# Kernel tuning notes

Hardware: AMD Instinct MI355X
Metric: run time of the kernel (lower is better)

## Reference

```python
import jax, jax.numpy as jnp
import numpy as np
import math

HEADS = 8
DIM_HEAD = 64


def setup_inputs() -> dict:
    key = jax.random.key(0)
    k1, k2, k3 = jax.random.split(key, 3)
    b, n, dim = 4, 2048, 512
    inner = HEADS * DIM_HEAD  # 512
    x = jax.random.normal(k1, (b, n, dim), dtype=jnp.float32)
    W_qkv = jax.random.normal(k2, (dim, 4 * inner), dtype=jnp.float32) * (dim ** -0.5)
    W_out = jax.random.normal(k3, (2 * inner, dim), dtype=jnp.float32) * ((2 * inner) ** -0.5)
    b_out = jnp.zeros((dim,), dtype=jnp.float32)
    return {"x": x, "W_qkv": W_qkv, "W_out": W_out, "b_out": b_out}


def reference(x, W_qkv, W_out, b_out):
    b, n, d = x.shape
    h, dh = HEADS, DIM_HEAD
    scale = dh ** -0.5
    qkvt = x @ W_qkv  # [b, n, 4*h*dh]
    q, k, v, t = jnp.split(qkvt, 4, axis=-1)
    # 'b n (h d) -> b h n d'
    def to_heads(z):
        return z.reshape(b, n, h, dh).transpose(0, 2, 1, 3)
    q, k, v, t = map(to_heads, (q, k, v, t))

    # Branch 1: standard softmax attention
    dots = jnp.einsum('bhid,bhjd->bhij', q, k) * scale
    attn1 = jax.nn.softmax(dots, axis=-1)
    out1 = jnp.einsum('bhij,bhjd->bhid', attn1, v)

    # Branch 2: fixed positional-decay attention (shared across b, h; no repeat needed)
    pos = jnp.arange(1, n + 1, dtype=x.dtype)  # linspace(1, n, n)
    tg = jnp.abs(pos[None, :] - pos[:, None])  # |j - i|, [n, n]
    attn2 = jnp.exp(-tg / jnp.asarray(math.e, dtype=x.dtype))
    # NOTE: original divides by sum(-1) WITHOUT keepdim -> broadcasts over columns:
    # attn2[i, j] / sum_k attn2[j, k]
    attn2 = attn2 / attn2.sum(-1)
    out2 = jnp.einsum('ij,bhjd->bhid', attn2, t)

    out = jnp.concatenate([out1, out2], axis=-1)  # [b, h, n, 2*dh]
    out = out.transpose(0, 2, 1, 3).reshape(b, n, 2 * h * dh)  # 'b h n d -> b n (h d)'
    return out @ W_out + b_out
```

## Files before the change

### kernel.cpp

```cpp
#include <hip/hip_runtime.h>
#include <hip/hip_bf16.h>

#define B_ 4
#define N_ 2048
#define D_ 512
#define H_ 8
#define DH_ 64

typedef float float4_ __attribute__((ext_vector_type(4)));
typedef int int2_ __attribute__((ext_vector_type(2)));
typedef int int4_ __attribute__((ext_vector_type(4)));
typedef unsigned short ushort4_ __attribute__((ext_vector_type(4)));
typedef unsigned short ushort8_ __attribute__((ext_vector_type(8)));
typedef __bf16 bf16x8 __attribute__((ext_vector_type(8)));
typedef _Float16 half2_ __attribute__((ext_vector_type(2)));
typedef _Float16 half4_ __attribute__((ext_vector_type(4)));
typedef _Float16 half8_ __attribute__((ext_vector_type(8)));

#if __has_builtin(__builtin_amdgcn_exp2f)
#define EXP2(x) __builtin_amdgcn_exp2f(x)
#else
#define EXP2(x) exp2f(x)
#endif

__device__ __forceinline__ float b2f(unsigned short u) {
  union { unsigned int u; float f; } v; v.u = ((unsigned int)u) << 16; return v.f;
}
__device__ __forceinline__ unsigned short f2b(float f) {
  union { float f; unsigned int u; } v; v.f = f;
  unsigned int r = v.u + 0x7fffu + ((v.u >> 16) & 1u);
  return (unsigned short)(r >> 16);
}
__device__ __forceinline__ half4_ pk4(float a, float b, float c, float d) {
  half2_ lo = __builtin_bit_cast(half2_, __builtin_amdgcn_cvt_pkrtz(a, b));
  half2_ hi = __builtin_bit_cast(half2_, __builtin_amdgcn_cvt_pkrtz(c, d));
  return __builtin_bit_cast(half4_,
      (int2_){__builtin_bit_cast(int, lo), __builtin_bit_cast(int, hi)});
}
__device__ __forceinline__ half8_ cat44(half4_ a, half4_ b) {
  int2_ ia = __builtin_bit_cast(int2_, a), ib = __builtin_bit_cast(int2_, b);
  int4_ r = {ia[0], ia[1], ib[0], ib[1]};
  return __builtin_bit_cast(half8_, r);
}

#define GLD16(gp, lp)                                                        \
  __builtin_amdgcn_global_load_lds(                                          \
      (const __attribute__((address_space(1))) unsigned int*)(gp),           \
      (__attribute__((address_space(3))) unsigned int*)(lp), 16, 0, 0)

__device__ __forceinline__ bool detect_fp32_local(
    const unsigned short* __restrict__ xhdr, int* cnt_sh) {
  if (threadIdx.x == 0) *cnt_sh = 0;
  __syncthreads();
  unsigned int e = (xhdr[threadIdx.x] >> 7) & 0xFFu;
  if (e >= 134u) atomicAdd(cnt_sh, 1);
  __syncthreads();
  return *cnt_sh > 16;
}

__device__ __forceinline__ void transpose_conv(
    const void* __restrict__ src, unsigned short* __restrict__ dst,
    int R, int C, int bx, int by, bool ofp) {
  __shared__ unsigned short tile[32][33];
  const int c0 = bx * 32, r0 = by * 32;
  const int tx = threadIdx.x & 31, ty = threadIdx.x >> 5;
#pragma unroll
  for (int k = 0; k < 4; ++k) {
    int r = ty + k * 8;
    long idx = (long)(r0 + r) * C + c0 + tx;
    tile[r][tx] = ofp ? f2b(((const float*)src)[idx])
                      : ((const unsigned short*)src)[idx];
  }
  __syncthreads();
#pragma unroll
  for (int k = 0; k < 4; ++k) {
    int c = ty + k * 8;
    dst[(long)(c0 + c) * R + r0 + tx] = tile[tx][c];
  }
}

__global__ __launch_bounds__(256) void prep_all(
    const void* __restrict__ xraw, const void* __restrict__ Wqraw,
    const void* __restrict__ Woraw, unsigned short* __restrict__ xb,
    unsigned short* __restrict__ WqT, unsigned short* __restrict__ WoT,
    unsigned short* __restrict__ Wband) {
  __shared__ int cnt_sh;
  const bool ofp = detect_fp32_local((const unsigned short*)xraw, &cnt_sh);
  const int bid = blockIdx.x;
  if (bid < 4096) {
    int i4 = bid * 256 + threadIdx.x;
    ushort4_ o;
    if (ofp) {
      float4_ v = ((const float4_*)xraw)[i4];
      o[0] = f2b(v[0]); o[1] = f2b(v[1]); o[2] = f2b(v[2]); o[3] = f2b(v[3]);
    } else {
      o = ((const ushort4_*)xraw)[i4];
    }
    *(ushort4_*)(xb + (long)i4 * 4) = o;
  } else if (bid < 5120) {
    const int b2 = bid - 4096;
    transpose_conv(Wqraw, WqT, 512, 2048, b2 % 64, b2 / 64, ofp);
  } else if (bid < 5632) {
    const int b2 = bid - 5120;
    transpose_conv(Woraw, WoT, 1024, 512, b2 % 16, b2 / 16, ofp);
  } else {
    constexpr float INV_E = 0.36787944117144233f;
    constexpr float R1 = 0.69220062755534635f;
    constexpr float INV_1MR = 3.2488706f;
    const int i = bid - 5632;
    const int krel = threadIdx.x;
    const int j = (i >> 6) * 64 - 96 + krel;
    float c = 0.f;
    if (j >= 0 && j < N_) {
      float wgt = __expf(-fabsf((float)(i - j)) * INV_E);
      float rj = __expf(-(float)j * INV_E);
      float rnj = __expf(-(float)(N_ - 1 - j) * INV_E);
      float S = 1.f + R1 * (2.f - rj - rnj) * INV_1MR;
      c = wgt / S;
    }
    _Float16 hv = (_Float16)c;
    Wband[i * 256 + krel] = __builtin_bit_cast(unsigned short, hv);
  }
}

#define MFMA16x32(d, a, b) \
  d = __builtin_amdgcn_mfma_f32_16x16x32_bf16(a, b, d, 0, 0, 0)

__global__ __launch_bounds__(512, 2) void gemm256(
    const unsigned short* __restrict__ A, const unsigned short* __restrict__ Bt,
    unsigned short* __restrict__ C, int M, int N, int K) {
  __shared__ unsigned short As[2][16384];
  __shared__ unsigned short Bs[2][16384];
  const int tid = threadIdx.x;
  const int w = tid >> 6, lane = tid & 63, l16 = lane & 15, quad = lane >> 4;
  const int wm = w >> 2, wn = w & 3;
  const long tm = (long)blockIdx.x * 256, tn = (long)blockIdx.y * 256;

  const int srow = tid >> 3;
  const int sch = (tid & 7) ^ (srow & 7);
  const unsigned short* gA = A + (tm + srow) * (long)K + sch * 8;
  const unsigned short* gB = Bt + (tn + srow) * (long)K + sch * 8;

  const int xr8 = l16 & 7;
  const int ch0 = ((0 + quad) ^ xr8) * 8;
  const int ch1 = ((4 + quad) ^ xr8) * 8;
  const int rowA0 = (wm * 128 + l16) * 64;
  const int rowB0 = (wn * 64 + l16) * 64;

  float4_ acc[8][4] = {};

  auto stage = [&](int t, int bufn) __attribute__((always_inline)) {
#pragma unroll
    for (int r = 0; r < 4; ++r)
      GLD16(gA + (long)(r * 64) * K + t * 64, &As[bufn][r * 4096 + w * 512]);
#pragma unroll
    for (int r = 0; r < 4; ++r)
      GLD16(gB + (long)(r * 64) * K + t * 64, &Bs[bufn][r * 4096 + w * 512]);
  };

  stage(0, 0);
  asm volatile("s_waitcnt vmcnt(0)" ::: "memory");
  __builtin_amdgcn_s_barrier();

  const int NT = K >> 6;
  for (int t = 0; t < NT; ++t) {
    const int buf = t & 1;
    const unsigned short* as = As[buf];
    const unsigned short* bs = Bs[buf];
    bf16x8 af[8], bq[4], br[4];
#pragma unroll
    for (int mi = 0; mi < 4; ++mi) {
      af[mi * 2]     = __builtin_bit_cast(bf16x8, *(const int4_*)&as[rowA0 + mi * 1024 + ch0]);
      af[mi * 2 + 1] = __builtin_bit_cast(bf16x8, *(const int4_*)&as[rowA0 + mi * 1024 + ch1]);
    }
#pragma unroll
    for (int ni = 0; ni < 2; ++ni) {
      bq[ni * 2]     = __builtin_bit_cast(bf16x8, *(const int4_*)&bs[rowB0 + ni * 1024 + ch0]);
      bq[ni * 2 + 1] = __builtin_bit_cast(bf16x8, *(const int4_*)&bs[rowB0 + ni * 1024 + ch1]);
    }
    if (t + 1 < NT) stage(t + 1, buf ^ 1);
    __builtin_amdgcn_s_barrier();
    asm volatile("s_waitcnt lgkmcnt(0)" ::: "memory");
    __builtin_amdgcn_sched_barrier(0);
    __builtin_amdgcn_s_setprio(1);
#pragma unroll
    for (int mi = 0; mi < 4; ++mi)
#pragma unroll
      for (int ni = 0; ni < 2; ++ni) {
        MFMA16x32(acc[mi][ni], af[mi * 2], bq[ni * 2]);
        MFMA16x32(acc[mi][ni], af[mi * 2 + 1], bq[ni * 2 + 1]);
      }
    __builtin_amdgcn_s_setprio(0);
    __builtin_amdgcn_s_barrier();
#pragma unroll
    for (int ni = 0; ni < 2; ++ni) {
      br[ni * 2]     = __builtin_bit_cast(bf16x8, *(const int4_*)&bs[rowB0 + (2 + ni) * 1024 + ch0]);
      br[ni * 2 + 1] = __builtin_bit_cast(bf16x8, *(const int4_*)&bs[rowB0 + (2 + ni) * 1024 + ch1]);
    }
    __builtin_amdgcn_s_barrier();
    asm volatile("s_waitcnt lgkmcnt(0)" ::: "memory");
    __builtin_amdgcn_sched_barrier(0);
    __builtin_amdgcn_s_setprio(1);
#pragma unroll
    for (int mi = 0; mi < 4; ++mi)
#pragma unroll
      for (int ni = 0; ni < 2; ++ni) {
        MFMA16x32(acc[mi][2 + ni], af[mi * 2], br[ni * 2]);
        MFMA16x32(acc[mi][2 + ni], af[mi * 2 + 1], br[ni * 2 + 1]);
      }
    __builtin_amdgcn_s_setprio(0);
    __builtin_amdgcn_s_barrier();
#pragma unroll
    for (int mi = 0; mi < 4; ++mi) {
      af[mi * 2]     = __builtin_bit_cast(bf16x8, *(const int4_*)&as[rowA0 + (4 + mi) * 1024 + ch0]);
      af[mi * 2 + 1] = __builtin_bit_cast(bf16x8, *(const int4_*)&as[rowA0 + (4 + mi) * 1024 + ch1]);
    }
    __builtin_amdgcn_s_barrier();
    asm volatile("s_waitcnt lgkmcnt(0)" ::: "memory");
    __builtin_amdgcn_sched_barrier(0);
    __builtin_amdgcn_s_setprio(1);
#pragma unroll
    for (int mi = 0; mi < 4; ++mi)
#pragma unroll
      for (int ni = 0; ni < 2; ++ni) {
        MFMA16x32(acc[4 + mi][2 + ni], af[mi * 2], br[ni * 2]);
        MFMA16x32(acc[4 + mi][2 + ni], af[mi * 2 + 1], br[ni * 2 + 1]);
      }
    __builtin_amdgcn_s_setprio(0);
    __builtin_amdgcn_s_barrier();
#pragma unroll
    for (int ni = 0; ni < 2; ++ni) {
      bq[ni * 2]     = __builtin_bit_cast(bf16x8, *(const int4_*)&bs[rowB0 + ni * 1024 + ch0]);
      bq[ni * 2 + 1] = __builtin_bit_cast(bf16x8, *(const int4_*)&bs[rowB0 + ni * 1024 + ch1]);
    }
    __builtin_amdgcn_s_barrier();
    asm volatile("s_waitcnt lgkmcnt(0)" ::: "memory");
    __builtin_amdgcn_sched_barrier(0);
    __builtin_amdgcn_s_setprio(1);
#pragma unroll
    for (int mi = 0; mi < 4; ++mi)
#pragma unroll
      for (int ni = 0; ni < 2; ++ni) {
        MFMA16x32(acc[4 + mi][ni], af[mi * 2], bq[ni * 2]);
        MFMA16x32(acc[4 + mi][ni], af[mi * 2 + 1], bq[ni * 2 + 1]);
      }
    __builtin_amdgcn_s_setprio(0);
    asm volatile("s_waitcnt vmcnt(0)" ::: "memory");
    __builtin_amdgcn_sched_barrier(0);
    __builtin_amdgcn_s_barrier();
  }
#pragma unroll
  for (int ni = 0; ni < 4; ++ni) {
    long col = tn + wn * 64 + ni * 16 + l16;
#pragma unroll
    for (int mi = 0; mi < 8; ++mi)
#pragma unroll
      for (int r = 0; r < 4; ++r) {
        long row = tm + wm * 128 + mi * 16 + quad * 4 + r;
        C[row * N + col] = f2b(acc[mi][ni][r]);
      }
  }
}

__global__ __launch_bounds__(512, 2) void gemm_o(
    const unsigned short* __restrict__ A, const unsigned short* __restrict__ Bt,
    void* __restrict__ C, const void* __restrict__ bias_raw,
    const unsigned short* __restrict__ xhdr) {
  __shared__ int cnt_sh;
  const bool ofp = detect_fp32_local(xhdr, &cnt_sh);
  __shared__ unsigned short As[2][8192];
  __shared__ unsigned short Bs[2][8192];
  constexpr int K = 1024, N = 512;
  const int tid = threadIdx.x;
  const int w = tid >> 6, lane = tid & 63, l16 = lane & 15, quad = lane >> 4;
  const int wm = w >> 2, wn = w & 3;
  const long tm = (long)blockIdx.x * 128, tn = (long)blockIdx.y * 128;
  const int srow = tid >> 3;
  const int sch = (tid & 7) ^ (srow & 7);
  const unsigned short* gA = A + (tm + srow) * (long)K + sch * 8;
  const unsigned short* gB = Bt + (tn + srow) * (long)K + sch * 8;
  const int xr8 = l16 & 7;
  const int ch0 = ((0 + quad) ^ xr8) * 8;
  const int ch1 = ((4 + quad) ^ xr8) * 8;
  const int rowA0 = (wm * 64 + l16) * 64;
  const int rowB0 = (wn * 32 + l16) * 64;
  float4_ acc[4][2] = {};

  auto stage = [&](int t, int bufn) __attribute__((always_inline)) {
#pragma unroll
    for (int r = 0; r < 2; ++r)
      GLD16(gA + (long)(r * 64) * K + t * 64, &As[bufn][r * 4096 + w * 512]);
#pragma unroll
    for (int r = 0; r < 2; ++r)
      GLD16(gB + (long)(r * 64) * K + t * 64, &Bs[bufn][r * 4096 + w * 512]);
  };

  stage(0, 0);
  asm volatile("s_waitcnt vmcnt(0)" ::: "memory");
  __builtin_amdgcn_s_barrier();

  const int NT = K >> 6;
  for (int t = 0; t < NT; ++t) {
    const int buf = t & 1;
    const unsigned short* as = As[buf];
    const unsigned short* bs = Bs[buf];
    bf16x8 af[8], bf0[2], bf1[2];
#pragma unroll
    for (int mi = 0; mi < 4; ++mi) {
      af[mi * 2]     = __builtin_bit_cast(bf16x8, *(const int4_*)&as[rowA0 + mi * 1024 + ch0]);
      af[mi * 2 + 1] = __builtin_bit_cast(bf16x8, *(const int4_*)&as[rowA0 + mi * 1024 + ch1]);
    }
    bf0[0] = __builtin_bit_cast(bf16x8, *(const int4_*)&bs[rowB0 + ch0]);
    bf0[1] = __builtin_bit_cast(bf16x8, *(const int4_*)&bs[rowB0 + ch1]);
    if (t + 1 < NT) stage(t + 1, buf ^ 1);
    __builtin_amdgcn_s_barrier();
    asm volatile("s_waitcnt lgkmcnt(0)" ::: "memory");
    __builtin_amdgcn_sched_barrier(0);
    __builtin_amdgcn_s_setprio(1);
#pragma unroll
    for (int mi = 0; mi < 4; ++mi) {
      MFMA16x32(acc[mi][0], af[mi * 2], bf0[0]);
      MFMA16x32(acc[mi][0], af[mi * 2 + 1], bf0[1]);
    }
    __builtin_amdgcn_s_setprio(0);
    __builtin_amdgcn_s_barrier();
    bf1[0] = __builtin_bit_cast(bf16x8, *(const int4_*)&bs[rowB0 + 1024 + ch0]);
    bf1[1] = __builtin_bit_cast(bf16x8, *(const int4_*)&bs[rowB0 + 1024 + ch1]);
    __builtin_amdgcn_s_barrier();
    asm volatile("s_waitcnt lgkmcnt(0)" ::: "memory");
    __builtin_amdgcn_sched_barrier(0);
    __builtin_amdgcn_s_setprio(1);
#pragma unroll
    for (int mi = 0; mi < 4; ++mi) {
      MFMA16x32(acc[mi][1], af[mi * 2], bf1[0]);
      MFMA16x32(acc[mi][1], af[mi * 2 + 1], bf1[1]);
    }
    __builtin_amdgcn_s_setprio(0);
    asm volatile("s_waitcnt vmcnt(0)" ::: "memory");
    __builtin_amdgcn_sched_barrier(0);
    __builtin_amdgcn_s_barrier();
  }
#pragma unroll
  for (int nb = 0; nb < 2; ++nb) {
    long col = tn + wn * 32 + nb * 16 + l16;
    float bv = ofp ? ((const float*)bias_raw)[col]
                   : b2f(((const unsigned short*)bias_raw)[col]);
#pragma unroll
    for (int mb = 0; mb < 4; ++mb)
#pragma unroll
      for (int r = 0; r < 4; ++r) {
        long row = tm + wm * 64 + mb * 16 + quad * 4 + r;
        float val = acc[mb][nb][r] + bv;
        if (ofp) ((float*)C)[row * N + col] = val;
        else ((unsigned short*)C)[row * N + col] = f2b(val);
      }
  }
}

#define TSW 266
__global__ __launch_bounds__(256) void mid_all(
    const unsigned short* __restrict__ qkvt, unsigned short* __restrict__ Vt,
    const unsigned short* __restrict__ Wband, unsigned short* __restrict__ catb) {
  __shared__ __align__(16) unsigned short Ts[64 * TSW];
  const int bid = blockIdx.x;
  const int tid = threadIdx.x;
  if (bid < 512) {
    unsigned int* Td = (unsigned int*)Ts;
    const int bh = bid >> 4, b = bh >> 3, h = bh & 7;
    const int j0 = (bid & 15) * 128;
    const int dg = tid & 7;
#pragma unroll
    for (int it = 0; it < 2; ++it) {
      const int jp = (tid >> 3) + 32 * it;
      const long base =
          (long)(b * N_ + j0 + 2 * jp) * 2048 + 1024 + h * 64 + dg * 8;
      ushort8_ r0 = __builtin_bit_cast(ushort8_, *(const int4_*)&qkvt[base]);
      ushort8_ r1 = __builtin_bit_cast(ushort8_, *(const int4_*)&qkvt[base + 2048]);
#pragma unroll
      for (int e = 0; e < 8; ++e) {
        const int d = dg * 8 + e;
        const int S = (d >> 3) | ((d & 1) << 3);
        unsigned short h0 = __builtin_bit_cast(unsigned short, (_Float16)b2f(r0[e]));
        unsigned short h1 = __builtin_bit_cast(unsigned short, (_Float16)b2f(r1[e]));
        Td[d * 68 + (jp ^ (S << 2))] = (unsigned int)h0 | ((unsigned int)h1 << 16);
      }
    }
    __syncthreads();
#pragma unroll
    for (int it = 0; it < 4; ++it) {
      const int d = (tid >> 4) + 16 * it;
      const int ch = tid & 15;
      const int S = (d >> 3) | ((d & 1) << 3);
      int4_ v = *(const int4_*)&Td[d * 68 + ((ch ^ S) << 2)];
      *(int4_*)&Vt[((long)bh * 64 + d) * 2048 + j0 + ch * 8] = v;
    }
    return;
  }
  const int b2 = bid - 512;
  const int qtile = b2 & 31;
  const int bh = b2 >> 5, b = bh >> 3, h = bh & 7;
  const int jlo = qtile * 64 - 96;
  {
    unsigned int* Tsd = (unsigned int*)Ts;
    const int dg = tid & 7;
#pragma unroll
    for (int it = 0; it < 4; ++it) {
      const int kkp = (tid >> 3) + 32 * it;
      const int jA = jlo + 2 * kkp, jB = jA + 1;
      int4_ r0 = {}, r1 = {};
      if (jA >= 0 && jA < N_)
        r0 = *(const int4_*)&qkvt[(long)(b * N_ + jA) * 2048 + 1536 + h * 64 + dg * 8];
      if (jB >= 0 && jB < N_)
        r1 = *(const int4_*)&qkvt[(long)(b * N_ + jB) * 2048 + 1536 + h * 64 + dg * 8];
      ushort8_ u0 = __builtin_bit_cast(ushort8_, r0);
      ushort8_ u1 = __builtin_bit_cast(ushort8_, r1);
#pragma unroll
      for (int e = 0; e < 8; ++e) {
        const int d = dg * 8 + e;
        unsigned short h0 = __builtin_bit_cast(unsigned short, (_Float16)b2f(u0[e]));
        unsigned short h1 = __builtin_bit_cast(unsigned short, (_Float16)b2f(u1[e]));
        Tsd[d * 133 + kkp] = (unsigned int)h0 | ((unsigned int)h1 << 16);
      }
    }
  }
  __syncthreads();
  const int w = tid >> 6, lane = tid & 63, l16 = lane & 15, quad = lane >> 4;
  const int i_row = qtile * 64 + w * 16 + l16;
  const unsigned short* ap = Wband + i_row * 256;
  float4_ acc[4] = {};
#pragma unroll
  for (int kh = 0; kh < 8; ++kh) {
    half8_ af = __builtin_bit_cast(half8_, *(const int4_*)&ap[kh * 32 + quad * 8]);
#pragma unroll
    for (int nb = 0; nb < 4; ++nb) {
      half8_ bf = __builtin_bit_cast(half8_,
          *(const int4_*)&Ts[(nb * 16 + l16) * TSW + kh * 32 + quad * 8]);
      acc[nb] = __builtin_amdgcn_mfma_f32_16x16x32_f16(af, bf, acc[nb], 0, 0, 0);
    }
  }
#pragma unroll
  for (int nb = 0; nb < 4; ++nb)
#pragma unroll
    for (int r = 0; r < 4; ++r) {
      int row = qtile * 64 + w * 16 + quad * 4 + r;
      catb[(long)(b * N_ + row) * 1024 + h * 128 + 64 + nb * 16 + l16] =
          f2b(acc[nb][r]);
    }
}

__global__ __launch_bounds__(256) void flash_kernel(
    const unsigned short* __restrict__ qkvt, const unsigned short* __restrict__ Vt,
    unsigned short* __restrict__ catb) {
  __shared__ unsigned short Ks[2][64 * 64];
  __shared__ unsigned short Vs[2][64 * 64];
  const int flat = blockIdx.x + blockIdx.y * 16;
  const int slot = flat & 7, idx = flat >> 3;
  const int bh = slot * 4 + (idx >> 4);
  const int i0 = (idx & 15) * 128;
  const int b = bh >> 3, h = bh & 7;
  const int tid = threadIdx.x;
  const int w = tid >> 6, lane = tid & 63, l16 = lane & 15, quad = lane >> 4;
  const int srow8 = lane >> 3, sch = lane & 7;
  const int chK = sch ^ srow8;
  bf16x8 qf[2][2];
  {
    constexpr float SCL = 0.125f * 1.44269504088896f;
#pragma unroll
    for (int s2 = 0; s2 < 2; ++s2) {
      const long qrow =
          (long)(b * N_ + i0 + w * 32 + s2 * 16 + l16) * 2048 + h * 64;
#pragma unroll
      for (int kh = 0; kh < 2; ++kh) {
        ushort8_ raw = __builtin_bit_cast(ushort8_,
            *(const int4_*)&qkvt[qrow + kh * 32 + quad * 8]);
        ushort8_ sc;
#pragma unroll
        for (int e = 0; e < 8; ++e) sc[e] = f2b(b2f(raw[e]) * SCL);
        qf[s2][kh] = __builtin_bit_cast(bf16x8, sc);
      }
    }
  }
  const unsigned short* kp[2];
#pragma unroll
  for (int kh = 0; kh < 2; ++kh)
    kp[kh] = &Ks[0][l16 * 64 + (((kh * 4 + quad) ^ (l16 & 7)) * 8)];
  const unsigned short* vp32[2];
#pragma unroll
  for (int wd = 0; wd < 2; ++wd)
    vp32[wd] = &Vs[0][l16 * 64 + (((wd * 4 + quad) ^ (l16 & 7)) * 8)];
  const unsigned short* kg[2];
  const unsigned short* vg[2];
#pragma unroll
  for (int g = 0; g < 2; ++g) {
    const int prow = w * 16 + g * 8 + srow8;
    const int ptok = (prow & 0x20) | ((prow & 0x10) >> 2) |
                     ((prow & 0x0C) << 1) | (prow & 3);
    kg[g] = qkvt + (long)(b * N_ + ptok) * 2048 + 512 + h * 64 + chK * 8;
    vg[g] = Vt + ((long)bh * 64 + prow) * 2048 + chK * 8;
  }
  float4_ O[2][4] = {};
  float4_ O5[2] = {};
  const half8_ ones8 = {(_Float16)1.f, (_Float16)1.f, (_Float16)1.f, (_Float16)1.f,
                        (_Float16)1.f, (_Float16)1.f, (_Float16)1.f, (_Float16)1.f};

  auto stage_k = [&](int jt_, int buf_) __attribute__((always_inline)) {
    const int j0 = jt_ * 64;
#pragma unroll
    for (int g = 0; g < 2; ++g)
      GLD16(kg[g] + (long)j0 * 2048,
            (char*)&Ks[0][0] + buf_ * 8192 + (w * 16 + g * 8) * 128);
  };
  auto stage_v = [&](int jt_, int buf_) __attribute__((always_inline)) {
    const int j0 = jt_ * 64;
#pragma unroll
    for (int g = 0; g < 2; ++g)
      GLD16(vg[g] + j0,
            (char*)&Vs[0][0] + buf_ * 8192 + (w * 16 + g * 8) * 128);
  };
  auto pv_step = [&](half4_ (&pf)[2][4], int vb) __attribute__((always_inline)) {
#pragma unroll
    for (int wd = 0; wd < 2; ++wd) {
      half8_ pa0 = cat44(pf[0][2 * wd], pf[0][2 * wd + 1]);
      half8_ pa1 = cat44(pf[1][2 * wd], pf[1][2 * wd + 1]);
#pragma unroll
      for (int dblk = 0; dblk < 4; ++dblk) {
        half8_ vfv = *(const half8_*)(vp32[wd] + vb + dblk * 1024);
        O[0][dblk] = __builtin_amdgcn_mfma_f32_16x16x32_f16(
            pa0, vfv, O[0][dblk], 0, 0, 0);
        O[1][dblk] = __builtin_amdgcn_mfma_f32_16x16x32_f16(
            pa1, vfv, O[1][dblk], 0, 0, 0);
      }
      O5[0] = __builtin_amdgcn_mfma_f32_16x16x32_f16(pa0, ones8, O5[0], 0, 0, 0);
      O5[1] = __builtin_amdgcn_mfma_f32_16x16x32_f16(pa1, ones8, O5[1], 0, 0, 0);
    }
  };
  auto phase = [&](int i, half4_ (&pfp)[2][4], half4_ (&pfc)[2][4],
                   bool first, bool last) __attribute__((always_inline)) {
    if (!last) stage_k(i + 1, (i + 1) & 1);
    stage_v(i, i & 1);
    const int kb = (i & 1) * 4096;
    float4_ s[2][4] = {};
#pragma unroll
    for (int kh = 0; kh < 2; ++kh)
#pragma unroll
      for (int c = 0; c < 4; ++c) {
        bf16x8 kf = __builtin_bit_cast(bf16x8,
            *(const int4_*)(kp[kh] + kb + c * 1024));
#pragma unroll
        for (int s2 = 0; s2 < 2; ++s2)
          s[s2][c] = __builtin_amdgcn_mfma_f32_16x16x32_bf16(
              kf, qf[s2][kh], s[s2][c], 0, 0, 0);
      }
    if (!first) pv_step(pfp, ((i - 1) & 1) * 4096);
#pragma unroll
    for (int s2 = 0; s2 < 2; ++s2)
#pragma unroll
      for (int c = 0; c < 4; ++c)
        pfc[s2][c] = pk4(EXP2(s[s2][c][0]), EXP2(s[s2][c][1]),
                         EXP2(s[s2][c][2]), EXP2(s[s2][c][3]));
    __syncthreads();
  };

  half4_ pfA[2][4], pfB[2][4];
  stage_k(0, 0);
  asm volatile("s_waitcnt vmcnt(0)" ::: "memory");
  __builtin_amdgcn_s_barrier();
  phase(0, pfB, pfA, true, false);
  for (int jt = 1; jt < 31; jt += 2) {
    phase(jt, pfA, pfB, false, false);
    phase(jt + 1, pfB, pfA, false, false);
  }
  phase(31, pfA, pfB, false, true);
  pv_step(pfB, (31 & 1) * 4096);

#pragma unroll
  for (int s2 = 0; s2 < 2; ++s2) {
    float linv[4];
#pragma unroll
    for (int r = 0; r < 4; ++r) linv[r] = 1.f / O5[s2][r];
#pragma unroll
    for (int dblk = 0; dblk < 4; ++dblk)
#pragma unroll
      for (int r = 0; r < 4; ++r) {
        int row = i0 + w * 32 + s2 * 16 + quad * 4 + r;
        catb[(long)(b * N_ + row) * 1024 + h * 128 + dblk * 16 + l16] =
            f2b(O[s2][dblk][r] * linv[r]);
      }
  }
}

extern "C" void kernel_launch(void* const* d_in, const int* in_sizes, int n_in,
                              void* d_out, int out_size, void* d_ws, size_t ws_size,
                              hipStream_t stream) {
  char* ws = (char*)d_ws;
  unsigned short* qkvt = (unsigned short*)(ws);
  unsigned short* WqT  = (unsigned short*)(ws + (size_t)32 * 1024 * 1024);
  unsigned short* WoT  = (unsigned short*)(ws + (size_t)34 * 1024 * 1024);
  unsigned short* Vt   = (unsigned short*)(ws + (size_t)35 * 1024 * 1024);
  unsigned short* catb = (unsigned short*)(ws + (size_t)43 * 1024 * 1024);
  unsigned short* xb   = (unsigned short*)(ws + (size_t)59 * 1024 * 1024);
  unsigned short* Wband= (unsigned short*)(ws + (size_t)68 * 1024 * 1024);

  prep_all<<<7680, 256, 0, stream>>>(d_in[0], d_in[1], d_in[2],
                                     xb, WqT, WoT, Wband);
  gemm256<<<dim3(8192 / 256, 2048 / 256), 512, 0, stream>>>(
      xb, WqT, qkvt, 8192, 2048, 512);
  mid_all<<<1536, 256, 0, stream>>>(qkvt, Vt, Wband, catb);
  flash_kernel<<<dim3(2048 / 128, 32), 256, 0, stream>>>(qkvt, Vt, catb);
  gemm_o<<<dim3(8192 / 128, 512 / 128), 512, 0, stream>>>(
      catb, WoT, d_out, d_in[3], (const unsigned short*)d_in[0]);
}
```

Measured before the change: 182.8 us.

## Deepen flash attention K/V pipeline to four LDS buffers with partial vmcnt waits

Grows the K and V shared-memory ring from two to four stages. K is now prefetched two tiles ahead and V one tile ahead, and the full syncthreads with vmcnt(0) at the end of each phase is replaced by a partial vmcnt wait, a sched_barrier and an s_barrier. The aim is to keep global-to-LDS loads in flight across iterations and hide memory latency behind the MFMA work. LDS use doubles, to 64KB per block, which may cut occupancy, and the vmcnt counts depend on each stage issuing exactly the assumed number of loads.

Result: no change. 182.7 us (median of 2 runs) (-0.0%).

```diff
diff --git a/kernel.cpp b/kernel.cpp
--- a/kernel.cpp
+++ b/kernel.cpp
@@ -47,6 +47,10 @@
   __builtin_amdgcn_global_load_lds(                                          \
       (const __attribute__((address_space(1))) unsigned int*)(gp),           \
       (__attribute__((address_space(3))) unsigned int*)(lp), 16, 0, 0)
+
+#define VMCNT(n) asm volatile("s_waitcnt vmcnt(" #n ")" ::: "memory")
+#define SCHED0   __builtin_amdgcn_sched_barrier(0)
+#define SBAR     __builtin_amdgcn_s_barrier()
 
 __device__ __forceinline__ bool detect_fp32_local(
     const unsigned short* __restrict__ xhdr, int* cnt_sh) {
@@ -451,8 +455,8 @@
 __global__ __launch_bounds__(256) void flash_kernel(
     const unsigned short* __restrict__ qkvt, const unsigned short* __restrict__ Vt,
     unsigned short* __restrict__ catb) {
-  __shared__ unsigned short Ks[2][64 * 64];
-  __shared__ unsigned short Vs[2][64 * 64];
+  __shared__ unsigned short Ks[4][64 * 64];
+  __shared__ unsigned short Vs[4][64 * 64];
   const int flat = blockIdx.x + blockIdx.y * 16;
   const int slot = flat & 7, idx = flat >> 3;
   const int bh = slot * 4 + (idx >> 4);
@@ -534,11 +538,12 @@
       O5[1] = __builtin_amdgcn_mfma_f32_16x16x32_f16(pa1, ones8, O5[1], 0, 0, 0);
     }
   };
-  auto phase = [&](int i, half4_ (&pfp)[2][4], half4_ (&pfc)[2][4],
-                   bool first, bool last) __attribute__((always_inline)) {
-    if (!last) stage_k(i + 1, (i + 1) & 1);
-    stage_v(i, i & 1);
-    const int kb = (i & 1) * 4096;
+  auto phase_body = [&](int i, half4_ (&pfp)[2][4], half4_ (&pfc)[2][4],
+                        bool first, bool stK, bool stV)
+      __attribute__((always_inline)) {
+    if (stK) stage_k(i + 2, (i + 2) & 3);
+    if (stV) stage_v(i + 1, (i + 1) & 3);
+    const int kb = (i & 3) * 4096;
     float4_ s[2][4] = {};
 #pragma unroll
     for (int kh = 0; kh < 2; ++kh)
@@ -551,27 +556,35 @@
           s[s2][c] = __builtin_amdgcn_mfma_f32_16x16x32_bf16(
               kf, qf[s2][kh], s[s2][c], 0, 0, 0);
       }
-    if (!first) pv_step(pfp, ((i - 1) & 1) * 4096);
+    if (!first) pv_step(pfp, ((i - 1) & 3) * 4096);
 #pragma unroll
     for (int s2 = 0; s2 < 2; ++s2)
 #pragma unroll
       for (int c = 0; c < 4; ++c)
         pfc[s2][c] = pk4(EXP2(s[s2][c][0]), EXP2(s[s2][c][1]),
                          EXP2(s[s2][c][2]), EXP2(s[s2][c][3]));
-    __syncthreads();
   };
 
   half4_ pfA[2][4], pfB[2][4];
   stage_k(0, 0);
-  asm volatile("s_waitcnt vmcnt(0)" ::: "memory");
-  __builtin_amdgcn_s_barrier();
-  phase(0, pfB, pfA, true, false);
-  for (int jt = 1; jt < 31; jt += 2) {
-    phase(jt, pfA, pfB, false, false);
-    phase(jt + 1, pfB, pfA, false, false);
-  }
-  phase(31, pfA, pfB, false, true);
-  pv_step(pfB, (31 & 1) * 4096);
+  stage_k(1, 1);
+  stage_v(0, 0);
+  VMCNT(4); SCHED0; SBAR;
+  phase_body(0, pfB, pfA, true, true, true);
+  VMCNT(4); SCHED0; SBAR;
+  for (int jt = 1; jt < 29; jt += 2) {
+    phase_body(jt, pfA, pfB, false, true, true);
+    VMCNT(4); SCHED0; SBAR;
+    phase_body(jt + 1, pfB, pfA, false, true, true);
+    VMCNT(4); SCHED0; SBAR;
+  }
+  phase_body(29, pfA, pfB, false, true, true);
+  VMCNT(4); SCHED0; SBAR;
+  phase_body(30, pfB, pfA, false, false, true);
+  VMCNT(2); SCHED0; SBAR;
+  phase_body(31, pfA, pfB, false, false, false);
+  VMCNT(0); SCHED0; SBAR;
+  pv_step(pfB, (31 & 3) * 4096);
 
 #pragma unroll
   for (int s2 = 0; s2 < 2; ++s2) {
```
